# Kernel tuning notes

Hardware: AMD Instinct MI355X
Metric: run time of the kernel (lower is better)

## Reference

```python
import jax, jax.numpy as jnp
import numpy as np

EMBED = 512
QDIM = 512
VDIM = 512
SRC = 4096
BSZ = 64


def setup_inputs() -> dict:
    key = jax.random.key(0)
    ks = jax.random.split(key, 6)
    query = jax.random.normal(ks[0], (BSZ, QDIM), dtype=jnp.float32)
    value = jax.random.normal(ks[1], (SRC, BSZ, VDIM), dtype=jnp.float32)
    key_padding_mask = jnp.zeros((SRC, BSZ), dtype=bool)
    # params: torch init uniform(-0.1, 0.1); b=0, g=sqrt(1/embed)
    Wq = jax.random.uniform(ks[2], (EMBED, QDIM), minval=-0.1, maxval=0.1, dtype=jnp.float32)
    Wv = jax.random.uniform(ks[3], (EMBED, VDIM), minval=-0.1, maxval=0.1, dtype=jnp.float32)
    v = jax.random.uniform(ks[4], (EMBED,), minval=-0.1, maxval=0.1, dtype=jnp.float32)
    b = jnp.zeros((EMBED,), dtype=jnp.float32)
    g = jnp.full((1,), np.sqrt(1.0 / EMBED), dtype=jnp.float32)
    return {"query": query, "value": value, "key_padding_mask": key_padding_mask,
            "Wq": Wq, "Wv": Wv, "v": v, "b": b, "g": g}


def reference(query, value, key_padding_mask, Wq, Wv, v, b, g):
    # projected_query: [1, bsz, embed]; key: [src, bsz, embed]
    pq = (query @ Wq.T)[None, :, :]
    key = jnp.einsum('sbv,ev->sbe', value, Wv)
    normed_v = g * v / jnp.linalg.norm(v)  # [embed]
    # attn_scores: [src, bsz]
    attn_scores = jnp.einsum('e,sbe->sb', normed_v, jnp.tanh(pq + key + b))
    attn_scores = jnp.where(key_padding_mask, -jnp.inf, attn_scores)
    attn_scores = jax.nn.softmax(attn_scores, axis=0)
    # context: [bsz, value_dim]
    context = jnp.einsum('sb,sbv->bv', attn_scores, value)
    return (context, attn_scores, attn_scores)
```

## Files before the change

kernel.cpp:

```cpp
#include <hip/hip_runtime.h>
#include <hip/hip_bf16.h>
#include <math.h>

typedef __bf16 bf16x8 __attribute__((ext_vector_type(8)));
typedef float  f32x4  __attribute__((ext_vector_type(4)));

#define SRC 4096
#define BSZ 64
#define EMB 512

__global__ void prep_all(const float* __restrict__ query, const float* __restrict__ Wq,
                         const float* __restrict__ bias, const float* __restrict__ v,
                         const float* __restrict__ g, const float* __restrict__ Wv,
                         float* __restrict__ nv, float* __restrict__ pqb,
                         __bf16* __restrict__ wvpk) {
  __shared__ float sh[EMB];
  __shared__ float red[256];
  const int blk = blockIdx.x, t = threadIdx.x;
  if (blk == 0) {
    float a = v[t], b = v[t + 256];
    red[t] = a * a + b * b;
    __syncthreads();
    for (int o = 128; o > 0; o >>= 1) {
      if (t < o) red[t] += red[t + o];
      __syncthreads();
    }
    float scale = g[0] / sqrtf(red[0]);
    nv[t]       = a * scale;
    nv[t + 256] = b * scale;
  } else if (blk <= 128) {
    int tid  = (blk - 1) * 256 + t;
    int lane = tid & 63;
    int ks   = (tid >> 6) & 15;
    int nsub = tid >> 10;
    int e  = nsub * 16 + (lane & 15);
    int k0 = ks * 32 + (lane >> 4) * 8;
    const float* src = Wv + (size_t)e * EMB + k0;
    bf16x8 o;
#pragma unroll
    for (int j = 0; j < 8; ++j) o[j] = (__bf16)src[j];
    *reinterpret_cast<bf16x8*>(wvpk + (size_t)tid * 8) = o;
  } else {
    int bb = blk - 129;
    int b = bb >> 1;
    int e = (bb & 1) * 256 + t;
    sh[t]       = query[b * EMB + t];
    sh[t + 256] = query[b * EMB + t + 256];
    __syncthreads();
    const float* wr = Wq + (size_t)e * EMB;
    float a0 = 0.f, a1 = 0.f;
#pragma unroll 8
    for (int k = 0; k < EMB; k += 8) {
      float4 q0 = *reinterpret_cast<const float4*>(&sh[k]);
      float4 w0 = *reinterpret_cast<const float4*>(&wr[k]);
      float4 q1 = *reinterpret_cast<const float4*>(&sh[k + 4]);
      float4 w1 = *reinterpret_cast<const float4*>(&wr[k + 4]);
      a0 += q0.x * w0.x + q0.y * w0.y + q0.z * w0.z + q0.w * w0.w;
      a1 += q1.x * w1.x + q1.y * w1.y + q1.z * w1.z + q1.w * w1.w;
    }
    pqb[b * EMB + e] = a0 + a1 + bias[e];
  }
}

__global__ __launch_bounds__(512, 4)
void scores_kernel(const float* __restrict__ value, const float* __restrict__ pqb,
                   const float* __restrict__ nv, const __bf16* __restrict__ wvpk,
                   float* __restrict__ scoresT) {
  __shared__ __bf16 As[BSZ * EMB];
  __shared__ float red[8][BSZ];
  const int s = blockIdx.x;
  const int t = threadIdx.x;

  {
    const int row = t >> 3, sub = t & 7;
    const float* src = value + (size_t)s * (BSZ * EMB) + (size_t)row * EMB + sub * 8;
#pragma unroll
    for (int j = 0; j < 8; ++j) {
      float4 v0 = *reinterpret_cast<const float4*>(src + j * 64);
      float4 v1 = *reinterpret_cast<const float4*>(src + j * 64 + 4);
      int kgp = (sub + j * 8) ^ (row & 7);
      bf16x8 o;
      o[0] = (__bf16)v0.x; o[1] = (__bf16)v0.y; o[2] = (__bf16)v0.z; o[3] = (__bf16)v0.w;
      o[4] = (__bf16)v1.x; o[5] = (__bf16)v1.y; o[6] = (__bf16)v1.z; o[7] = (__bf16)v1.w;
      *reinterpret_cast<bf16x8*>(&As[row * EMB + kgp * 8]) = o;
    }
  }
  __syncthreads();

  const int w = t >> 6, l = t & 63, lr = l & 15, lk = l >> 4;

  f32x4 acc[4][4];
#pragma unroll
  for (int m = 0; m < 4; ++m)
#pragma unroll
    for (int n = 0; n < 4; ++n)
#pragma unroll
      for (int r = 0; r < 4; ++r) acc[m][n][r] = 0.f;

  const __bf16* bp = wvpk + (size_t)(w * 4) * 16 * 512 + (size_t)l * 8;
  bf16x8 bq[2][4];
#pragma unroll
  for (int n = 0; n < 4; ++n)
    bq[0][n] = *reinterpret_cast<const bf16x8*>(bp + (size_t)(n * 16) * 512);

#pragma unroll
  for (int ksg = 0; ksg < 16; ++ksg) {
    if (ksg < 15) {
#pragma unroll
      for (int n = 0; n < 4; ++n)
        bq[(ksg + 1) & 1][n] =
            *reinterpret_cast<const bf16x8*>(bp + (size_t)(n * 16 + ksg + 1) * 512);
    }
    const int kgp = ((ksg * 4 + lk) ^ (lr & 7)) * 8;
#pragma unroll
    for (int m = 0; m < 4; ++m) {
      bf16x8 a = *reinterpret_cast<const bf16x8*>(&As[(m * 16 + lr) * EMB + kgp]);
#pragma unroll
      for (int n = 0; n < 4; ++n)
        acc[m][n] = __builtin_amdgcn_mfma_f32_16x16x32_bf16(a, bq[ksg & 1][n], acc[m][n], 0, 0, 0);
    }
  }

  float sc[16];
#pragma unroll
  for (int i = 0; i < 16; ++i) sc[i] = 0.f;
#pragma unroll
  for (int n = 0; n < 4; ++n) {
    int col = w * 64 + n * 16 + lr;
    float nvc = nv[col];
#pragma unroll
    for (int m = 0; m < 4; ++m) {
#pragma unroll
      for (int r = 0; r < 4; ++r) {
        int brow = m * 16 + lk * 4 + r;
        float x = acc[m][n][r] + pqb[brow * EMB + col];
        float e = __expf(2.0f * x);
        float rcp = __builtin_amdgcn_rcpf(1.0f + e);
        sc[m * 4 + r] += fmaf(-2.0f * nvc, rcp, nvc);
      }
    }
  }

#pragma unroll
  for (int i = 0; i < 16; ++i) {
    float vsum = sc[i];
#pragma unroll
    for (int off = 1; off < 16; off <<= 1) vsum += __shfl_xor(vsum, off, 64);
    if (lr == 0) red[w][(i >> 2) * 16 + lk * 4 + (i & 3)] = vsum;
  }
  __syncthreads();
  if (t < BSZ) {
    float total = 0.f;
#pragma unroll
    for (int ww = 0; ww < 8; ++ww) total += red[ww][t];
    scoresT[(size_t)t * SRC + s] = total;
  }
}

__global__ void softmax_k(const float* __restrict__ scoresT, const unsigned char* __restrict__ mask,
                          float* __restrict__ pT, float* __restrict__ attn0,
                          float* __restrict__ attn1) {
  __shared__ float buf[SRC];
  __shared__ float red[256];
  int b = blockIdx.x, t = threadIdx.x;
  float mx = -1e30f;
  for (int s = t; s < SRC; s += 256) {
    float x = scoresT[(size_t)b * SRC + s];
    if (mask[(size_t)s * BSZ + b]) x = -1e30f;
    buf[s] = x;
    mx = fmaxf(mx, x);
  }
  red[t] = mx; __syncthreads();
  for (int o = 128; o > 0; o >>= 1) { if (t < o) red[t] = fmaxf(red[t], red[t + o]); __syncthreads(); }
  mx = red[0]; __syncthreads();
  float sum = 0.f;
  for (int s = t; s < SRC; s += 256) { float e = __expf(buf[s] - mx); buf[s] = e; sum += e; }
  red[t] = sum; __syncthreads();
  for (int o = 128; o > 0; o >>= 1) { if (t < o) red[t] += red[t + o]; __syncthreads(); }
  float inv = 1.0f / red[0];
  for (int s = t; s < SRC; s += 256) {
    float p = buf[s] * inv;
    pT[(size_t)b * SRC + s] = p;
    attn0[(size_t)s * BSZ + b] = p;
    attn1[(size_t)s * BSZ + b] = p;
  }
}

__global__ __launch_bounds__(256)
void ctx_partial(const float* __restrict__ value, const float* __restrict__ pT,
                 float* __restrict__ parts) {
  int blk = blockIdx.x;
  int c = blk >> 6;
  int b = blk & 63;
  int t = threadIdx.x;
  int f4 = t & 127, half = t >> 7;
  const float* pb = pT + (size_t)b * SRC + c * 256 + half;
  const float* vb = value + ((size_t)(c * 256 + half) * BSZ + b) * EMB + f4 * 4;
  float4 acc = make_float4(0.f, 0.f, 0.f, 0.f);
#pragma unroll 8
  for (int j = 0; j < 128; ++j) {
    float p = pb[j * 2];
    float4 vv = *reinterpret_cast<const float4*>(vb + (size_t)j * 2 * BSZ * EMB);
    acc.x += p * vv.x; acc.y += p * vv.y; acc.z += p * vv.z; acc.w += p * vv.w;
  }
  *reinterpret_cast<float4*>(parts + ((size_t)(c * 2 + half) * BSZ + b) * EMB + f4 * 4) = acc;
}

__global__ void ctx_reduce(const float* __restrict__ parts, float* __restrict__ out_ctx) {
  int idx = blockIdx.x * 256 + threadIdx.x;
  float acc = 0.f;
#pragma unroll
  for (int c = 0; c < 32; ++c) acc += parts[(size_t)c * (BSZ * EMB) + idx];
  out_ctx[idx] = acc;
}

extern "C" void kernel_launch(void* const* d_in, const int* in_sizes, int n_in,
                              void* d_out, int out_size, void* d_ws, size_t ws_size,
                              hipStream_t stream) {
  const float* query        = (const float*)d_in[0];
  const float* value        = (const float*)d_in[1];
  const unsigned char* mask = (const unsigned char*)d_in[2];
  const float* Wq           = (const float*)d_in[3];
  const float* Wv           = (const float*)d_in[4];
  const float* v            = (const float*)d_in[5];
  const float* bias         = (const float*)d_in[6];
  const float* g            = (const float*)d_in[7];

  float* out_ctx = (float*)d_out;
  float* attn0   = (float*)d_out + BSZ * EMB;
  float* attn1   = attn0 + SRC * BSZ;

  char* ws = (char*)d_ws;
  float*  nv      = (float*)(ws);
  float*  pqb     = (float*)(ws + 2048);
  __bf16* wvpk    = (__bf16*)(ws + 2048 + 131072);
  float*  scoresT = (float*)(ws + 2048 + 131072 + 524288);
  float*  pT      = scoresT + SRC * BSZ;
  float*  parts   = pT + SRC * BSZ;

  prep_all<<<257, 256, 0, stream>>>(query, Wq, bias, v, g, Wv, nv, pqb, wvpk);
  scores_kernel<<<SRC, 512, 0, stream>>>(value, pqb, nv, wvpk, scoresT);
  softmax_k<<<BSZ, 256, 0, stream>>>(scoresT, mask, pT, attn0, attn1);
  ctx_partial<<<BSZ * 16, 256, 0, stream>>>(value, pT, parts);
  ctx_reduce<<<128, 256, 0, stream>>>(parts, out_ctx);
}
```

Before: 969.5 us.

## Make scores kernel persistent over 8 source rows with register-prefetched value tiles

Each scores block now processes 8 source positions, two at a time, with a double-sized LDS tile. The next pair's fp32 value rows are prefetched into registers and converted to bf16 while the MFMA passes run, then written to LDS after a barrier. Warps are regrouped into a 2x4 M/N split so each Wv fragment load is reused across two source rows. The aim is to hide the global load latency and amortise Wv reads. In exchange it uses many more registers, drops occupancy to 2 blocks, and launches only 512 blocks.

```diff
diff --git a/kernel.cpp b/kernel.cpp
--- a/kernel.cpp
+++ b/kernel.cpp
@@ -8,6 +8,8 @@
 #define SRC 4096
 #define BSZ 64
 #define EMB 512
+#define SBLK 8
+#define PAIRS 4
 
 __global__ void prep_all(const float* __restrict__ query, const float* __restrict__ Wq,
                          const float* __restrict__ bias, const float* __restrict__ v,
@@ -62,98 +64,176 @@
   }
 }
 
-__global__ __launch_bounds__(512, 4)
+__global__ __launch_bounds__(512, 2)
 void scores_kernel(const float* __restrict__ value, const float* __restrict__ pqb,
                    const float* __restrict__ nv, const __bf16* __restrict__ wvpk,
                    float* __restrict__ scoresT) {
-  __shared__ __bf16 As[BSZ * EMB];
-  __shared__ float red[8][BSZ];
-  const int s = blockIdx.x;
-  const int t = threadIdx.x;
-
-  {
-    const int row = t >> 3, sub = t & 7;
-    const float* src = value + (size_t)s * (BSZ * EMB) + (size_t)row * EMB + sub * 8;
+  __shared__ __bf16 As[2][BSZ * EMB];
+  __shared__ float red[2][4][BSZ];
+  const int sb = blockIdx.x * SBLK;
+  const int t  = threadIdx.x;
+  const int row = t >> 3, sub = t & 7, swz = row & 7;
+
+#pragma unroll
+  for (int ss = 0; ss < 2; ++ss) {
+    const float* src = value + (size_t)(sb + ss) * (BSZ * EMB) + (size_t)row * EMB + sub * 8;
+    __bf16* dst = &As[ss][row * EMB];
 #pragma unroll
     for (int j = 0; j < 8; ++j) {
       float4 v0 = *reinterpret_cast<const float4*>(src + j * 64);
       float4 v1 = *reinterpret_cast<const float4*>(src + j * 64 + 4);
-      int kgp = (sub + j * 8) ^ (row & 7);
       bf16x8 o;
       o[0] = (__bf16)v0.x; o[1] = (__bf16)v0.y; o[2] = (__bf16)v0.z; o[3] = (__bf16)v0.w;
       o[4] = (__bf16)v1.x; o[5] = (__bf16)v1.y; o[6] = (__bf16)v1.z; o[7] = (__bf16)v1.w;
-      *reinterpret_cast<bf16x8*>(&As[row * EMB + kgp * 8]) = o;
+      *reinterpret_cast<bf16x8*>(dst + ((sub + j * 8) ^ swz) * 8) = o;
     }
   }
   __syncthreads();
 
   const int w = t >> 6, l = t & 63, lr = l & 15, lk = l >> 4;
-
-  f32x4 acc[4][4];
-#pragma unroll
-  for (int m = 0; m < 4; ++m)
-#pragma unroll
-    for (int n = 0; n < 4; ++n)
-#pragma unroll
-      for (int r = 0; r < 4; ++r) acc[m][n][r] = 0.f;
-
-  const __bf16* bp = wvpk + (size_t)(w * 4) * 16 * 512 + (size_t)l * 8;
-  bf16x8 bq[2][4];
-#pragma unroll
-  for (int n = 0; n < 4; ++n)
-    bq[0][n] = *reinterpret_cast<const bf16x8*>(bp + (size_t)(n * 16) * 512);
-
-#pragma unroll
-  for (int ksg = 0; ksg < 16; ++ksg) {
-    if (ksg < 15) {
-#pragma unroll
-      for (int n = 0; n < 4; ++n)
-        bq[(ksg + 1) & 1][n] =
-            *reinterpret_cast<const bf16x8*>(bp + (size_t)(n * 16 + ksg + 1) * 512);
-    }
-    const int kgp = ((ksg * 4 + lk) ^ (lr & 7)) * 8;
-#pragma unroll
-    for (int m = 0; m < 4; ++m) {
-      bf16x8 a = *reinterpret_cast<const bf16x8*>(&As[(m * 16 + lr) * EMB + kgp]);
-#pragma unroll
-      for (int n = 0; n < 4; ++n)
-        acc[m][n] = __builtin_amdgcn_mfma_f32_16x16x32_bf16(a, bq[ksg & 1][n], acc[m][n], 0, 0, 0);
-    }
-  }
-
-  float sc[16];
-#pragma unroll
-  for (int i = 0; i < 16; ++i) sc[i] = 0.f;
-#pragma unroll
-  for (int n = 0; n < 4; ++n) {
-    int col = w * 64 + n * 16 + lr;
-    float nvc = nv[col];
-#pragma unroll
-    for (int m = 0; m < 4; ++m) {
-#pragma unroll
-      for (int r = 0; r < 4; ++r) {
-        int brow = m * 16 + lk * 4 + r;
-        float x = acc[m][n][r] + pqb[brow * EMB + col];
-        float e = __expf(2.0f * x);
-        float rcp = __builtin_amdgcn_rcpf(1.0f + e);
-        sc[m * 4 + r] += fmaf(-2.0f * nvc, rcp, nvc);
-      }
-    }
-  }
-
-#pragma unroll
-  for (int i = 0; i < 16; ++i) {
-    float vsum = sc[i];
-#pragma unroll
-    for (int off = 1; off < 16; off <<= 1) vsum += __shfl_xor(vsum, off, 64);
-    if (lr == 0) red[w][(i >> 2) * 16 + lk * 4 + (i & 3)] = vsum;
-  }
-  __syncthreads();
-  if (t < BSZ) {
-    float total = 0.f;
-#pragma unroll
-    for (int ww = 0; ww < 8; ++ww) total += red[ww][t];
-    scoresT[(size_t)t * SRC + s] = total;
+  const int mg = w >> 2;
+  const int ng = w & 3;
+  const __bf16* bqw = wvpk + (size_t)(ng * 8) * 16 * 512 + (size_t)l * 8;
+
+  float sc[2][8];
+
+  auto run_pass = [&](int h) {
+    f32x4 acc[2][2][4];
+#pragma unroll
+    for (int s2 = 0; s2 < 2; ++s2)
+#pragma unroll
+      for (int mi = 0; mi < 2; ++mi)
+#pragma unroll
+        for (int n2 = 0; n2 < 4; ++n2)
+#pragma unroll
+          for (int r = 0; r < 4; ++r) acc[s2][mi][n2][r] = 0.f;
+    const __bf16* bph = bqw + (size_t)h * (4 * 16 * 512);
+    bf16x8 bq[2][4];
+#pragma unroll
+    for (int n2 = 0; n2 < 4; ++n2)
+      bq[0][n2] = *reinterpret_cast<const bf16x8*>(bph + (size_t)(n2 * 16) * 512);
+#pragma unroll
+    for (int ksg = 0; ksg < 16; ++ksg) {
+      if (ksg < 15) {
+#pragma unroll
+        for (int n2 = 0; n2 < 4; ++n2)
+          bq[(ksg + 1) & 1][n2] =
+              *reinterpret_cast<const bf16x8*>(bph + (size_t)(n2 * 16 + ksg + 1) * 512);
+      }
+      const int kgp = ((ksg * 4 + lk) ^ (lr & 7)) * 8;
+      bf16x8 a[2][2];
+#pragma unroll
+      for (int s2 = 0; s2 < 2; ++s2)
+#pragma unroll
+        for (int mi = 0; mi < 2; ++mi)
+          a[s2][mi] = *reinterpret_cast<const bf16x8*>(
+              &As[s2][((mg * 2 + mi) * 16 + lr) * EMB + kgp]);
+#pragma unroll
+      for (int s2 = 0; s2 < 2; ++s2)
+#pragma unroll
+        for (int mi = 0; mi < 2; ++mi)
+#pragma unroll
+          for (int n2 = 0; n2 < 4; ++n2)
+            acc[s2][mi][n2] = __builtin_amdgcn_mfma_f32_16x16x32_bf16(
+                a[s2][mi], bq[ksg & 1][n2], acc[s2][mi][n2], 0, 0, 0);
+    }
+#pragma unroll
+    for (int s2 = 0; s2 < 2; ++s2)
+#pragma unroll
+      for (int n2 = 0; n2 < 4; ++n2) {
+        const int col = (ng * 8 + h * 4 + n2) * 16 + lr;
+        const float nvc = nv[col];
+#pragma unroll
+        for (int mi = 0; mi < 2; ++mi)
+#pragma unroll
+          for (int r = 0; r < 4; ++r) {
+            const int brow = (mg * 2 + mi) * 16 + lk * 4 + r;
+            float x = acc[s2][mi][n2][r] + pqb[(size_t)brow * EMB + col];
+            float e = __expf(2.0f * x);
+            float rcp = __builtin_amdgcn_rcpf(1.0f + e);
+            sc[s2][mi * 4 + r] += fmaf(-2.0f * nvc, rcp, nvc);
+          }
+      }
+  };
+
+  for (int p = 0; p < PAIRS; ++p) {
+    float4 F2[16], F3[16];
+    bf16x8 H2[8], H3[8];
+    const bool pre = (p < PAIRS - 1);
+
+    if (pre) {
+      const float* src =
+          value + (size_t)(sb + 2 * p + 2) * (BSZ * EMB) + (size_t)row * EMB + sub * 8;
+#pragma unroll
+      for (int j = 0; j < 8; ++j) {
+        F2[2 * j]     = *reinterpret_cast<const float4*>(src + j * 64);
+        F2[2 * j + 1] = *reinterpret_cast<const float4*>(src + j * 64 + 4);
+      }
+    }
+#pragma unroll
+    for (int s2 = 0; s2 < 2; ++s2)
+#pragma unroll
+      for (int i = 0; i < 8; ++i) sc[s2][i] = 0.f;
+
+    run_pass(0);
+
+    if (pre) {
+#pragma unroll
+      for (int j = 0; j < 8; ++j) {
+        float4 v0 = F2[2 * j], v1 = F2[2 * j + 1];
+        H2[j][0] = (__bf16)v0.x; H2[j][1] = (__bf16)v0.y; H2[j][2] = (__bf16)v0.z; H2[j][3] = (__bf16)v0.w;
+        H2[j][4] = (__bf16)v1.x; H2[j][5] = (__bf16)v1.y; H2[j][6] = (__bf16)v1.z; H2[j][7] = (__bf16)v1.w;
+      }
+    }
+
+    run_pass(1);
+
+    if (pre) {
+      const float* src =
+          value + (size_t)(sb + 2 * p + 3) * (BSZ * EMB) + (size_t)row * EMB + sub * 8;
+#pragma unroll
+      for (int j = 0; j < 8; ++j) {
+        F3[2 * j]     = *reinterpret_cast<const float4*>(src + j * 64);
+        F3[2 * j + 1] = *reinterpret_cast<const float4*>(src + j * 64 + 4);
+      }
+    }
+
+#pragma unroll
+    for (int s2 = 0; s2 < 2; ++s2)
+#pragma unroll
+      for (int i = 0; i < 8; ++i) {
+        float vsum = sc[s2][i];
+        vsum += __shfl_xor(vsum, 1, 64);
+        vsum += __shfl_xor(vsum, 2, 64);
+        vsum += __shfl_xor(vsum, 4, 64);
+        vsum += __shfl_xor(vsum, 8, 64);
+        if (lr == 0) red[s2][ng][mg * 32 + (i >> 2) * 16 + lk * 4 + (i & 3)] = vsum;
+      }
+    __syncthreads();
+
+    if (pre) {
+#pragma unroll
+      for (int j = 0; j < 8; ++j) {
+        float4 v0 = F3[2 * j], v1 = F3[2 * j + 1];
+        H3[j][0] = (__bf16)v0.x; H3[j][1] = (__bf16)v0.y; H3[j][2] = (__bf16)v0.z; H3[j][3] = (__bf16)v0.w;
+        H3[j][4] = (__bf16)v1.x; H3[j][5] = (__bf16)v1.y; H3[j][6] = (__bf16)v1.z; H3[j][7] = (__bf16)v1.w;
+      }
+      __bf16* d0 = &As[0][row * EMB];
+      __bf16* d1 = &As[1][row * EMB];
+#pragma unroll
+      for (int j = 0; j < 8; ++j) {
+        const int off = ((sub + j * 8) ^ swz) * 8;
+        *reinterpret_cast<bf16x8*>(d0 + off) = H2[j];
+        *reinterpret_cast<bf16x8*>(d1 + off) = H3[j];
+      }
+    }
+    if (t < BSZ) {
+      float t0 = red[0][0][t] + red[0][1][t] + red[0][2][t] + red[0][3][t];
+      float t1 = red[1][0][t] + red[1][1][t] + red[1][2][t] + red[1][3][t];
+      scoresT[(size_t)t * SRC + (sb + 2 * p)]     = t0;
+      scoresT[(size_t)t * SRC + (sb + 2 * p + 1)] = t1;
+    }
+    __syncthreads();
   }
 }
 
@@ -239,7 +319,7 @@
   float*  parts   = pT + SRC * BSZ;
 
   prep_all<<<257, 256, 0, stream>>>(query, Wq, bias, v, g, Wv, nv, pqb, wvpk);
-  scores_kernel<<<SRC, 512, 0, stream>>>(value, pqb, nv, wvpk, scoresT);
+  scores_kernel<<<SRC / SBLK, 512, 0, stream>>>(value, pqb, nv, wvpk, scoresT);
   softmax_k<<<BSZ, 256, 0, stream>>>(scoresT, mask, pT, attn0, attn1);
   ctx_partial<<<BSZ * 16, 256, 0, stream>>>(value, pT, parts);
   ctx_reduce<<<128, 256, 0, stream>>>(parts, out_ctx);
```

After: 2.243 ms. 131% more time.
